# Kernel optimization log

Hardware: AMD Instinct MI355X
Metric: run time of the kernel (lower is better)

Reference implementation:

```python
import jax, jax.numpy as jnp
import numpy as np
from jax.scipy.linalg import expm

B, D, NF = 65536, 15, 199
DT, T_PERIOD, NORM = 0.05, 5.0, 150.0
TWO_PI = 2.0 * np.pi


def _pauli_s_const():
    # su(4) structure constants from normalized two-qubit Pauli basis G_a = (s_i x s_j)/2, Tr(Ga Gb)=delta
    I = np.eye(2, dtype=np.complex64)
    X = np.array([[0, 1], [1, 0]], np.complex64)
    Y = np.array([[0, -1j], [1j, 0]], np.complex64)
    Z = np.array([[1, 0], [0, -1]], np.complex64)
    P = [I, X, Y, Z]
    G = np.stack([np.kron(a, b) / 2.0 for i, a in enumerate(P) for j, b in enumerate(P) if (i, j) != (0, 0)])
    prod = np.einsum('aij,bjk->abik', G, G)
    comm = prod - prod.transpose(1, 0, 2, 3)
    anti = prod + prod.transpose(1, 0, 2, 3)
    f = np.real(-1j * np.einsum('abik,cki->abc', comm, G)).astype(np.float32)
    d = np.real(np.einsum('abik,cki->abc', anti, G)).astype(np.float32)
    return jnp.asarray(f), jnp.asarray(d)


def _fourier(t, freqs, amp):
    # FourierLayer: learnable frequencies + amplitudes, no phase; t: (B,1) -> (B, 2*NF)
    phase = TWO_PI * t * freqs / T_PERIOD  # (B, NF)
    return amp * jnp.concatenate([jnp.cos(phase), jnp.sin(phase)], axis=-1)


def setup_inputs() -> dict:
    key = jax.random.key(0)
    ks = jax.random.split(key, 12)
    t = jax.random.uniform(ks[0], (B, 1), jnp.float32) * T_PERIOD
    x = jax.random.normal(ks[1], (B, D), jnp.float32)
    # kaiming_uniform with a=10: bound = sqrt(6 / ((1 + a^2) * fan_in))
    bu = float(np.sqrt(6.0 / (101.0 * D)))
    u_re = jax.random.uniform(ks[2], (D, D), jnp.float32, -bu, bu)
    u_im = jax.random.uniform(ks[3], (D, D), jnp.float32, -bu, bu)
    freqs = jnp.arange(0.5, 100.0, 0.5, dtype=jnp.float32)  # (199,)
    bl = float(1.0 / np.sqrt(2 * NF))
    inp = {
        't': t, 'x': x, 'u_re': u_re, 'u_im': u_im,
        'freqs_g': freqs, 'amp_g': jnp.ones((2 * NF,), jnp.float32),
        'w_g': jax.random.uniform(ks[4], (D, 2 * NF), jnp.float32, -bl, bl),
        'b_g': jax.random.uniform(ks[5], (D,), jnp.float32, -bl, bl),
        'freqs_o': freqs, 'amp_o': jnp.ones((2 * NF,), jnp.float32),
        'w_o': jax.random.uniform(ks[6], (D, 2 * NF), jnp.float32, -bl, bl),
        'b_o': jax.random.uniform(ks[7], (D,), jnp.float32, -bl, bl),
    }
    f, d = _pauli_s_const()
    inp['f'] = f
    inp['d'] = d
    return inp


def reference(t, x, u_re, u_im, freqs_g, amp_g, w_g, b_g, freqs_o, amp_o, w_o, b_o, f, d):
    gamma = (( _fourier(t, freqs_g, amp_g) @ w_g.T + b_g) ** 2) / NORM   # (B, D), Square nonlin
    omega = (_fourier(t, freqs_o, amp_o) @ w_o.T + b_o) / NORM           # (B, D)
    # Hermitian theta -> unitary u = expm(i theta)
    theta = (u_re + u_re.T).astype(jnp.complex64) + 1j * (u_im - u_im.T).astype(jnp.complex64)
    u = expm(1j * theta)  # (D, D) complex64
    # Kossakowski matrix c = u diag(gamma) u^H, batched over samples
    c = jnp.einsum('ij,sj,lj->sil', u, gamma.astype(jnp.complex64), jnp.conj(u))
    c_re, c_im = c.real, c.imag
    dsx = (-4.0 * jnp.einsum('mjk,nik,sij->smn', f, f, c_re)
           - 4.0 * jnp.einsum('mik,njk,sij->smn', f, f, c_re)
           + 4.0 * jnp.einsum('mjk,nik,sij->smn', f, d, c_im)
           - 4.0 * jnp.einsum('mik,njk,sij->smn', f, d, c_im))
    tr_id = 4.0 * jnp.einsum('imj,sij->sm', f, c_im)
    h_comm = -4.0 * jnp.einsum('kij,sk->sij', f, omega)
    bsz = x.shape[0]
    L = jnp.zeros((bsz, D + 1, D + 1), jnp.float32)
    L = L.at[:, 1:, 1:].set(h_comm + dsx)
    L = L.at[:, 1:, 0].set(tr_id)
    E = jax.vmap(expm)(DT * L)  # batched 16x16 matrix exponential
    return E[:, 1:, 0] + jnp.einsum('si,sji->sj', x, E[:, 1:, 1:])
```

## Files before the change

### kernel.cpp

```cpp
#include <hip/hip_runtime.h>
#include <hip/hip_bf16.h>
#include <math.h>

#define NB      65536
#define DD      15
#define NFQ     199
#define DTC     0.05f
#define INV_NORM (1.0f/150.0f)
#define PH_SCALE 1.2566370614359172f
#define KTAY    10
#define KTAY_U  30

typedef _Float16 f16x8 __attribute__((ext_vector_type(8)));
typedef _Float16 f16x2 __attribute__((ext_vector_type(2)));
typedef float    f32x4 __attribute__((ext_vector_type(4)));

static __device__ __forceinline__ f16x2 u2h(unsigned u) {
    return __builtin_bit_cast(f16x2, u);
}
static __device__ __forceinline__ unsigned packh(float lo, float hi) {
    f16x2 h; h.x = (_Float16)lo; h.y = (_Float16)hi;
    return __builtin_bit_cast(unsigned, h);
}
static __device__ __forceinline__ f16x2 cvt_pk(float lo, float hi) {
    return __builtin_bit_cast(f16x2, __builtin_amdgcn_cvt_pkrtz(lo, hi));
}
static __device__ __forceinline__ float dot2(f16x2 cs, unsigned wbits, float acc) {
#if __has_builtin(__builtin_amdgcn_fdot2)
    return __builtin_amdgcn_fdot2(cs, u2h(wbits), acc, false);
#else
    f16x2 w = u2h(wbits);
    return acc + (float)cs.x * (float)w.x + (float)cs.y * (float)w.y;
#endif
}

__global__ __launch_bounds__(256) void k_pre(const float* __restrict__ u_re,
                                             const float* __restrict__ u_im,
                                             const float* __restrict__ ag,
                                             const float* __restrict__ wg,
                                             const float* __restrict__ ao,
                                             const float* __restrict__ wo,
                                             float* __restrict__ ws_u,
                                             unsigned* __restrict__ wt16) {
    int tid = threadIdx.x;
    if (blockIdx.x == 0) {
        __shared__ float Mre[225], Mim[225];
        __shared__ float cre[2][225], cim[2][225];
        float accre = 0.0f, accim = 0.0f;
        if (tid < 225) {
            int a = tid / 15, b = tid % 15;
            float tre = u_re[a*15+b] + u_re[b*15+a];
            float tim = u_im[a*15+b] - u_im[b*15+a];
            Mre[tid] = -tim;
            Mim[tid] =  tre;
            float id = (a == b) ? 1.0f : 0.0f;
            cre[0][tid] = id; cim[0][tid] = 0.0f;
            accre = id;
        }
        __syncthreads();
        int cur = 0;
        for (int k = 1; k <= KTAY_U; ++k) {
            float nre = 0.0f, nim = 0.0f;
            if (tid < 225) {
                int a = tid / 15, b = tid % 15;
                for (int j = 0; j < 15; ++j) {
                    float mre = Mre[a*15+j], mim = Mim[a*15+j];
                    float xre = cre[cur][j*15+b], xim = cim[cur][j*15+b];
                    nre += mre*xre - mim*xim;
                    nim += mre*xim + mim*xre;
                }
                float inv = 1.0f / (float)k;
                nre *= inv; nim *= inv;
                cre[cur^1][tid] = nre; cim[cur^1][tid] = nim;
                accre += nre; accim += nim;
            }
            __syncthreads();
            cur ^= 1;
        }
        if (tid < 225) {
            ws_u[2*tid]   = accre;
            ws_u[2*tid+1] = accim;
        }
    } else {
        int n = blockIdx.x - 1;
        if (tid < 32) {
            unsigned v = 0u;
            if (n < NFQ) {
                if (tid < 15) {
                    v = packh(wg[tid*398 + n] * ag[n],
                              wg[tid*398 + 199 + n] * ag[199 + n]);
                } else if (tid >= 16 && tid < 31) {
                    int m = tid - 16;
                    v = packh(wo[m*398 + n] * ao[n],
                              wo[m*398 + 199 + n] * ao[199 + n]);
                }
            }
            wt16[n*36 + tid] = v;
        }
    }
}

extern __shared__ float smem[];

__global__ __launch_bounds__(256) void k_mid(const float* __restrict__ f,
                                             const float* __restrict__ dten,
                                             const float* __restrict__ ws_u,
                                             const float* __restrict__ t,
                                             const float* __restrict__ bg,
                                             const float* __restrict__ bo,
                                             const unsigned* __restrict__ wt16,
                                             _Float16* __restrict__ Lb16,
                                             unsigned* __restrict__ coef16) {
    int tid = threadIdx.x;
    if (blockIdx.x < 16) {
        int p = blockIdx.x;
        int c = tid >> 4, r = tid & 15;
        if (p == 15) {
            Lb16[c*512 + r*32 + 15] = (_Float16)0.0f;
            Lb16[c*512 + r*32 + 31] = (_Float16)0.0f;
            return;
        }
        float* fsp  = smem;
        float* dshp = smem + 3600;
        float* FRt  = smem + 7200;
        float* DIt  = smem + 10800;
        float* Rm   = smem + 14400;
        float* Im   = smem + 14625;
        float* accA = smem + 14850;
        float* colv = smem + 15075;
        float* sur  = smem + 15090;
        float* sui  = smem + 15105;

        for (int idx = tid; idx < 3600; idx += 256) {
            int k = idx & 15, ab = idx >> 4;
            float fv = 0.0f, dv = 0.0f;
            if (k < 15) { fv = f[ab*15 + k]; dv = dten[ab*15 + k]; }
            fsp[idx] = fv; dshp[idx] = dv;
        }
        if (tid < 15) {
            sur[tid] = ws_u[2*(tid*15 + p)];
            sui[tid] = ws_u[2*(tid*15 + p) + 1];
        }
        __syncthreads();

        if (tid < 225) {
            int i = tid / 15, j = tid % 15;
            Rm[tid] = sur[i]*sur[j] + sui[i]*sui[j];
            Im[tid] = sui[i]*sur[j] - sur[i]*sui[j];
        }
        __syncthreads();

        for (int idx = tid; idx < 3600; idx += 256) {
            int k  = idx & 15;
            int nj = idx >> 4;
            int n  = nj / 15;
            int j  = nj % 15;
            float s1 = 0.0f, s2 = 0.0f;
            if (k < 15) {
                for (int i = 0; i < 15; ++i)  s1 += fsp[(n*15+i)*16 + k] * Rm[i*15 + j];
                for (int jj = 0; jj < 15; ++jj) s2 += dshp[(n*15+jj)*16 + k] * Im[j*15 + jj];
            }
            FRt[idx] = s1;
            DIt[idx] = s2;
        }
        __syncthreads();

        if (tid < 225) {
            int m = tid / 15, n = tid % 15;
            float acc = 0.0f;
            for (int j = 0; j < 15; ++j) {
                const float* fa = &fsp[(m*15+j)*16];
                const float* fb = &FRt[(n*15+j)*16];
                const float* fc = &DIt[(n*15+j)*16];
#pragma unroll
                for (int kk = 0; kk < 4; ++kk) {
                    float4 a4 = *(const float4*)(fa + 4*kk);
                    float4 b4 = *(const float4*)(fb + 4*kk);
                    float4 c4 = *(const float4*)(fc + 4*kk);
                    acc += a4.x*(b4.x + c4.x) + a4.y*(b4.y + c4.y)
                         + a4.z*(b4.z + c4.z) + a4.w*(b4.w + c4.w);
                }
            }
            accA[tid] = -8.0f * acc;
        }
        if (tid < 15) {
            int m = tid;
            float s = 0.0f;
            for (int i = 0; i < 15; ++i)
                for (int j = 0; j < 15; ++j)
                    s += fsp[(i*15+m)*16 + j] * Im[i*15 + j];
            colv[m] = 4.0f * s;
        }
        __syncthreads();

        float vg, vo;
        if (r == 0)      { vg = 0.0f;                      vo = 0.0f; }
        else if (c == 0) { vg = colv[r-1];                 vo = 0.0f; }
        else             { vg = accA[(r-1)*15 + (c-1)];
                           vo = -4.0f * fsp[(p*15 + (r-1))*16 + (c-1)]; }
        Lb16[c*512 + r*32 + p]      = (_Float16)vg;
        Lb16[c*512 + r*32 + 16 + p] = (_Float16)vo;
    } else {
        unsigned* lw = (unsigned*)smem;
        for (int idx = tid; idx < 200*32; idx += 256) {
            int n = idx >> 5, tt = idx & 31;
            lw[n*36 + tt] = wt16[n*36 + tt];
        }
        __syncthreads();

        int q = tid & 3;
        int p = tid >> 2;
        int sbase = (blockIdx.x - 16) * 256 + p;

        float rc[4], rs[4], rc4[4], rs4[4];
#pragma unroll
        for (int i = 0; i < 4; ++i) {
            float d = 0.5f * PH_SCALE * t[sbase + 64*i];
            __sincosf((float)(q + 1) * d, &rs[i], &rc[i]);
            __sincosf(4.0f * d, &rs4[i], &rc4[i]);
        }

        float ga[4][15], oa[4][15];
#pragma unroll
        for (int i = 0; i < 4; ++i)
#pragma unroll
            for (int m = 0; m < 15; ++m) { ga[i][m] = 0.0f; oa[i][m] = 0.0f; }

#pragma unroll 1
        for (int k = 0; k < 50; ++k) {
            const uint4* rowv = (const uint4*)(lw + (4*k + q) * 36);
            unsigned us[32];
#pragma unroll
            for (int j = 0; j < 8; ++j) {
                uint4 a_ = rowv[j];
                us[4*j] = a_.x; us[4*j+1] = a_.y; us[4*j+2] = a_.z; us[4*j+3] = a_.w;
            }
#pragma unroll
            for (int i = 0; i < 4; ++i) {
                f16x2 cs = cvt_pk(rc[i], rs[i]);
#pragma unroll
                for (int m = 0; m < 15; ++m) {
                    ga[i][m] = dot2(cs, us[m],      ga[i][m]);
                    oa[i][m] = dot2(cs, us[16 + m], oa[i][m]);
                }
                float cn = rc[i]*rc4[i] - rs[i]*rs4[i];
                float sn = rs[i]*rc4[i] + rc[i]*rs4[i];
                rc[i] = cn; rs[i] = sn;
            }
        }

#pragma unroll
        for (int i = 0; i < 4; ++i)
#pragma unroll
            for (int m = 0; m < 15; ++m) {
                ga[i][m] += __shfl_xor(ga[i][m], 1, 64);
                ga[i][m] += __shfl_xor(ga[i][m], 2, 64);
                oa[i][m] += __shfl_xor(oa[i][m], 1, 64);
                oa[i][m] += __shfl_xor(oa[i][m], 2, 64);
            }

        float bgv[15], bov[15];
#pragma unroll
        for (int m = 0; m < 15; ++m) { bgv[m] = bg[m]; bov[m] = bo[m]; }

#pragma unroll
        for (int i = 0; i < 4; ++i) {
            float rv[32];
#pragma unroll
            for (int m = 0; m < 15; ++m) {
                float g = ga[i][m] + bgv[m];
                rv[m]      = g * g * INV_NORM;
                rv[16 + m] = (oa[i][m] + bov[m]) * INV_NORM;
            }
            rv[15] = 0.0f; rv[31] = 0.0f;
            unsigned u0  = packh(rv[0],  rv[1]),  u1  = packh(rv[2],  rv[3]);
            unsigned u2  = packh(rv[4],  rv[5]),  u3  = packh(rv[6],  rv[7]);
            unsigned u4  = packh(rv[8],  rv[9]),  u5  = packh(rv[10], rv[11]);
            unsigned u6  = packh(rv[12], rv[13]), u7  = packh(rv[14], rv[15]);
            unsigned u8  = packh(rv[16], rv[17]), u9  = packh(rv[18], rv[19]);
            unsigned u10 = packh(rv[20], rv[21]), u11 = packh(rv[22], rv[23]);
            unsigned u12 = packh(rv[24], rv[25]), u13 = packh(rv[26], rv[27]);
            unsigned u14 = packh(rv[28], rv[29]), u15 = packh(rv[30], rv[31]);
            uint4 wr;
            if      (q == 0) wr = make_uint4(u0,  u1,  u2,  u3);
            else if (q == 1) wr = make_uint4(u4,  u5,  u6,  u7);
            else if (q == 2) wr = make_uint4(u8,  u9,  u10, u11);
            else             wr = make_uint4(u12, u13, u14, u15);
            *(uint4*)(coef16 + (size_t)(sbase + 64*i) * 16 + 4*q) = wr;
        }
    }
}

__global__ __launch_bounds__(256) void k_main(const float* __restrict__ x,
                                              const unsigned* __restrict__ coef16,
                                              const _Float16* __restrict__ Lb16,
                                              float* __restrict__ out) {
    __shared__ float wl[4 * 16 * 20];
    int tid  = threadIdx.x;
    int wave = tid >> 6, lane = tid & 63;
    int grp  = lane >> 4, sl = lane & 15;
    int s    = blockIdx.x * 64 + wave * 16 + sl;

    f16x8 bh = *(const f16x8*)((const _Float16*)coef16 + (size_t)s * 32 + grp * 8);

    f32x4 acc[16];
    f32x4 zero4 = {0.0f, 0.0f, 0.0f, 0.0f};
#pragma unroll
    for (int c = 0; c < 16; ++c) {
        f16x8 af = *(const f16x8*)(Lb16 + c*512 + sl*32 + grp*8);
        acc[c] = __builtin_amdgcn_mfma_f32_16x16x32_f16(af, bh, zero4, 0, 0, 0);
    }

    float4 wv;
    if (grp == 0) {
        const float* xp = x + (size_t)s * 15;
        wv = make_float4(1.0f, xp[0], xp[1], xp[2]);
    } else {
        const float* xp = x + (size_t)s * 15 + 4*grp - 1;
        wv = make_float4(xp[0], xp[1], xp[2], xp[3]);
    }
    float4 accv = wv;

    float* slot = wl + wave*320 + sl*20;
#pragma unroll
    for (int k = 1; k <= KTAY; ++k) {
        *(float4*)(slot + 4*grp) = wv;
        float wz[16];
        {
            float4 a = *(const float4*)(slot + 0);
            wz[0]=a.x; wz[1]=a.y; wz[2]=a.z; wz[3]=a.w;
            float4 b = *(const float4*)(slot + 4);
            wz[4]=b.x; wz[5]=b.y; wz[6]=b.z; wz[7]=b.w;
            float4 c = *(const float4*)(slot + 8);
            wz[8]=c.x; wz[9]=c.y; wz[10]=c.z; wz[11]=c.w;
            float4 d = *(const float4*)(slot + 12);
            wz[12]=d.x; wz[13]=d.y; wz[14]=d.z; wz[15]=d.w;
        }
        float nx = 0.0f, ny = 0.0f, nz = 0.0f, nw = 0.0f;
#pragma unroll
        for (int c = 0; c < 16; ++c) {
            f32x4 A = acc[c];
            float wc = wz[c];
            nx += A.x * wc; ny += A.y * wc; nz += A.z * wc; nw += A.w * wc;
        }
        float sc = DTC / (float)k;
        wv = make_float4(nx*sc, ny*sc, nz*sc, nw*sc);
        accv.x += wv.x; accv.y += wv.y; accv.z += wv.z; accv.w += wv.w;
    }

    float* op = out + (size_t)s * 15 - 1;
    int row = 4 * grp;
    if (row > 0)     op[row]     = accv.x;
    op[row + 1] = accv.y;
    op[row + 2] = accv.z;
    op[row + 3] = accv.w;
}

extern "C" void kernel_launch(void* const* d_in, const int* in_sizes, int n_in,
                              void* d_out, int out_size, void* d_ws, size_t ws_size,
                              hipStream_t stream) {
    const float* t    = (const float*)d_in[0];
    const float* x    = (const float*)d_in[1];
    const float* u_re = (const float*)d_in[2];
    const float* u_im = (const float*)d_in[3];
    const float* ag   = (const float*)d_in[5];
    const float* wg   = (const float*)d_in[6];
    const float* bg   = (const float*)d_in[7];
    const float* ao   = (const float*)d_in[9];
    const float* wo   = (const float*)d_in[10];
    const float* bo   = (const float*)d_in[11];
    const float* f    = (const float*)d_in[12];
    const float* dten = (const float*)d_in[13];
    float* out = (float*)d_out;
    float* ws  = (float*)d_ws;

    float*     u_ws   = ws;
    _Float16*  Lb16   = (_Float16*)(ws + 512);
    unsigned*  wt16   = (unsigned*)(ws + 4608);
    unsigned*  coef16 = (unsigned*)(ws + 12288);

    hipLaunchKernelGGL(k_pre,  dim3(201),  dim3(256), 0,     stream,
                       u_re, u_im, ag, wg, ao, wo, u_ws, wt16);
    hipLaunchKernelGGL(k_mid,  dim3(272),  dim3(256), 60480, stream,
                       f, dten, u_ws, t, bg, bo, wt16, Lb16, coef16);
    hipLaunchKernelGGL(k_main, dim3(1024), dim3(256), 0,     stream,
                       x, coef16, Lb16, out);
}
```

Before: 140.8 us.

## Fuse three kernels into one cooperative kernel with a grid-wide sync

Replaces the three-launch pipeline (pre, mid, main) with a single cooperative kernel of 256 blocks. The first 16 blocks each compute the unitary exponential redundantly, with the Taylor order cut from 30 to 18, and then build the generator matrices from fp16-packed structure constants. The remaining blocks build the Fourier weights in shared memory and loop over sample chunks to compute the coefficients. After a grid.sync, every block runs the batched MFMA Taylor exponential for its 256 samples, so launch gaps and intermediate workspace round trips go away. In exchange the grid is smaller and stalls at the grid barrier. Fewer Taylor terms and fp16 constants also add precision risk, and the old three kernels are kept as a fallback if the cooperative launch fails.

```diff
diff --git a/kernel.cpp b/kernel.cpp
--- a/kernel.cpp
+++ b/kernel.cpp
@@ -1,15 +1,17 @@
 #include <hip/hip_runtime.h>
+#include <hip/hip_cooperative_groups.h>
 #include <hip/hip_bf16.h>
 #include <math.h>
 
+namespace cg = cooperative_groups;
+
 #define NB      65536
-#define DD      15
 #define NFQ     199
 #define DTC     0.05f
 #define INV_NORM (1.0f/150.0f)
 #define PH_SCALE 1.2566370614359172f
 #define KTAY    10
-#define KTAY_U  30
+#define KTAY_U  18
 
 typedef _Float16 f16x8 __attribute__((ext_vector_type(8)));
 typedef _Float16 f16x2 __attribute__((ext_vector_type(2)));
@@ -32,6 +34,307 @@
     f16x2 w = u2h(wbits);
     return acc + (float)cs.x * (float)w.x + (float)cs.y * (float)w.y;
 #endif
+}
+
+extern __shared__ float sm[];
+
+__global__ __launch_bounds__(256) void k_all(
+        const float* __restrict__ t,   const float* __restrict__ x,
+        const float* __restrict__ u_re,const float* __restrict__ u_im,
+        const float* __restrict__ ag,  const float* __restrict__ wg,
+        const float* __restrict__ bg,  const float* __restrict__ ao,
+        const float* __restrict__ wo,  const float* __restrict__ bo,
+        const float* __restrict__ f,   const float* __restrict__ dten,
+        _Float16* __restrict__ Lb16,   unsigned* __restrict__ coef16,
+        float* __restrict__ out) {
+    int tid = threadIdx.x;
+    int bid = blockIdx.x;
+
+    if (bid < 16) {
+        if (bid == 15) {
+            int c = tid >> 4, r = tid & 15;
+            Lb16[c*512 + r*32 + 15] = (_Float16)0.0f;
+            Lb16[c*512 + r*32 + 31] = (_Float16)0.0f;
+        } else {
+            int p = bid;
+            unsigned* fd16 = (unsigned*)sm;
+            float* S    = sm + 3600;
+            float* Rm   = sm + 7200;
+            float* Im   = sm + 7425;
+            float* accA = sm + 7650;
+            float* colv = sm + 7875;
+            float* sur  = sm + 7890;
+            float* sui  = sm + 7905;
+            float* Mre  = sm + 3600;
+            float* Mim  = sm + 3825;
+            float* creb = sm + 4050;
+            float* cimb = sm + 4500;
+
+            for (int idx = tid; idx < 3600; idx += 256) {
+                int k = idx & 15, ab = idx >> 4;
+                float fv = 0.0f, dv = 0.0f;
+                if (k < 15) { fv = f[ab*15 + k]; dv = dten[ab*15 + k]; }
+                fd16[idx] = packh(fv, dv);
+            }
+            float accre = 0.0f, accim = 0.0f;
+            if (tid < 225) {
+                int a = tid / 15, b = tid % 15;
+                float tre = u_re[a*15+b] + u_re[b*15+a];
+                float tim = u_im[a*15+b] - u_im[b*15+a];
+                Mre[tid] = -tim;
+                Mim[tid] =  tre;
+                float id = (a == b) ? 1.0f : 0.0f;
+                creb[tid] = id; cimb[tid] = 0.0f;
+                accre = id;
+            }
+            __syncthreads();
+            int cur = 0;
+            for (int k = 1; k <= KTAY_U; ++k) {
+                float nre = 0.0f, nim = 0.0f;
+                if (tid < 225) {
+                    int a = tid / 15, b = tid % 15;
+                    for (int j = 0; j < 15; ++j) {
+                        float mre = Mre[a*15+j], mim = Mim[a*15+j];
+                        float xre = creb[cur*225 + j*15+b], xim = cimb[cur*225 + j*15+b];
+                        nre += mre*xre - mim*xim;
+                        nim += mre*xim + mim*xre;
+                    }
+                    float inv = 1.0f / (float)k;
+                    nre *= inv; nim *= inv;
+                    creb[(cur^1)*225 + tid] = nre; cimb[(cur^1)*225 + tid] = nim;
+                    accre += nre; accim += nim;
+                }
+                __syncthreads();
+                cur ^= 1;
+            }
+            if (tid < 225 && (tid % 15) == p) { sur[tid/15] = accre; sui[tid/15] = accim; }
+            __syncthreads();
+            if (tid < 225) {
+                int i = tid / 15, j = tid % 15;
+                Rm[tid] = sur[i]*sur[j] + sui[i]*sui[j];
+                Im[tid] = sui[i]*sur[j] - sur[i]*sui[j];
+            }
+            __syncthreads();
+            for (int idx = tid; idx < 3600; idx += 256) {
+                int k  = idx & 15;
+                int nj = idx >> 4;
+                int n  = nj / 15;
+                int j  = nj % 15;
+                float s1 = 0.0f, s2 = 0.0f;
+                if (k < 15) {
+                    for (int i = 0; i < 15; ++i) {
+                        f16x2 fd = u2h(fd16[(n*15+i)*16 + k]);
+                        s1 += (float)fd.x * Rm[i*15 + j];
+                        s2 += (float)fd.y * Im[j*15 + i];
+                    }
+                }
+                S[idx] = s1 + s2;
+            }
+            __syncthreads();
+            if (tid < 225) {
+                int m = tid / 15, n = tid % 15;
+                float acc = 0.0f;
+                for (int j = 0; j < 15; ++j) {
+                    const unsigned* fa = &fd16[(m*15+j)*16];
+                    const float*    fs = &S   [(n*15+j)*16];
+                    for (int k = 0; k < 15; ++k) {
+                        f16x2 fd = u2h(fa[k]);
+                        acc += (float)fd.x * fs[k];
+                    }
+                }
+                accA[tid] = -8.0f * acc;
+            }
+            if (tid < 15) {
+                int m = tid;
+                float s = 0.0f;
+                for (int i = 0; i < 15; ++i)
+                    for (int j = 0; j < 15; ++j) {
+                        f16x2 fd = u2h(fd16[(i*15+m)*16 + j]);
+                        s += (float)fd.x * Im[i*15 + j];
+                    }
+                colv[m] = 4.0f * s;
+            }
+            __syncthreads();
+            {
+                int c = tid >> 4, r = tid & 15;
+                float vg, vo;
+                if (r == 0)      { vg = 0.0f;              vo = 0.0f; }
+                else if (c == 0) { vg = colv[r-1];         vo = 0.0f; }
+                else             { vg = accA[(r-1)*15 + (c-1)];
+                                   f16x2 fd = u2h(fd16[(p*15 + (r-1))*16 + (c-1)]);
+                                   vo = -4.0f * (float)fd.x; }
+                Lb16[c*512 + r*32 + p]      = (_Float16)vg;
+                Lb16[c*512 + r*32 + 16 + p] = (_Float16)vo;
+            }
+        }
+    } else {
+        unsigned* lw = (unsigned*)sm;
+        for (int idx = tid; idx < 200*36; idx += 256) lw[idx] = 0u;
+        __syncthreads();
+        for (int idx = tid; idx < 15*200; idx += 256) {
+            int m = idx / 200, n = idx % 200;
+            if (n < NFQ)
+                lw[n*36 + m] = packh(wg[m*398 + n]       * ag[n],
+                                     wg[m*398 + 199 + n] * ag[199 + n]);
+        }
+        for (int idx = tid; idx < 15*200; idx += 256) {
+            int m = idx / 200, n = idx % 200;
+            if (n < NFQ)
+                lw[n*36 + 16 + m] = packh(wo[m*398 + n]       * ao[n],
+                                          wo[m*398 + 199 + n] * ao[199 + n]);
+        }
+        __syncthreads();
+
+        int q = tid & 3;
+        int pp = tid >> 2;
+
+        float bgv[15], bov[15];
+#pragma unroll
+        for (int m = 0; m < 15; ++m) { bgv[m] = bg[m]; bov[m] = bo[m]; }
+
+        for (int cb = bid - 16; cb < 256; cb += 240) {
+            int sbase = cb * 256 + pp;
+
+            float rc[4], rs[4], rc4[4], rs4[4];
+#pragma unroll
+            for (int i = 0; i < 4; ++i) {
+                float d = 0.5f * PH_SCALE * t[sbase + 64*i];
+                __sincosf((float)(q + 1) * d, &rs[i], &rc[i]);
+                __sincosf(4.0f * d, &rs4[i], &rc4[i]);
+            }
+
+            float ga[4][15], oa[4][15];
+#pragma unroll
+            for (int i = 0; i < 4; ++i)
+#pragma unroll
+                for (int m = 0; m < 15; ++m) { ga[i][m] = 0.0f; oa[i][m] = 0.0f; }
+
+#pragma unroll 1
+            for (int k = 0; k < 50; ++k) {
+                const uint4* rowv = (const uint4*)(lw + (4*k + q) * 36);
+                unsigned us[32];
+#pragma unroll
+                for (int j = 0; j < 8; ++j) {
+                    uint4 a_ = rowv[j];
+                    us[4*j] = a_.x; us[4*j+1] = a_.y; us[4*j+2] = a_.z; us[4*j+3] = a_.w;
+                }
+#pragma unroll
+                for (int i = 0; i < 4; ++i) {
+                    f16x2 cs = cvt_pk(rc[i], rs[i]);
+#pragma unroll
+                    for (int m = 0; m < 15; ++m) {
+                        ga[i][m] = dot2(cs, us[m],      ga[i][m]);
+                        oa[i][m] = dot2(cs, us[16 + m], oa[i][m]);
+                    }
+                    float cn = rc[i]*rc4[i] - rs[i]*rs4[i];
+                    float sn = rs[i]*rc4[i] + rc[i]*rs4[i];
+                    rc[i] = cn; rs[i] = sn;
+                }
+            }
+
+#pragma unroll
+            for (int i = 0; i < 4; ++i)
+#pragma unroll
+                for (int m = 0; m < 15; ++m) {
+                    ga[i][m] += __shfl_xor(ga[i][m], 1, 64);
+                    ga[i][m] += __shfl_xor(ga[i][m], 2, 64);
+                    oa[i][m] += __shfl_xor(oa[i][m], 1, 64);
+                    oa[i][m] += __shfl_xor(oa[i][m], 2, 64);
+                }
+
+#pragma unroll
+            for (int i = 0; i < 4; ++i) {
+                float rv[32];
+#pragma unroll
+                for (int m = 0; m < 15; ++m) {
+                    float g = ga[i][m] + bgv[m];
+                    rv[m]      = g * g * INV_NORM;
+                    rv[16 + m] = (oa[i][m] + bov[m]) * INV_NORM;
+                }
+                rv[15] = 0.0f; rv[31] = 0.0f;
+                unsigned u0  = packh(rv[0],  rv[1]),  u1  = packh(rv[2],  rv[3]);
+                unsigned u2  = packh(rv[4],  rv[5]),  u3  = packh(rv[6],  rv[7]);
+                unsigned u4  = packh(rv[8],  rv[9]),  u5  = packh(rv[10], rv[11]);
+                unsigned u6  = packh(rv[12], rv[13]), u7  = packh(rv[14], rv[15]);
+                unsigned u8  = packh(rv[16], rv[17]), u9  = packh(rv[18], rv[19]);
+                unsigned u10 = packh(rv[20], rv[21]), u11 = packh(rv[22], rv[23]);
+                unsigned u12 = packh(rv[24], rv[25]), u13 = packh(rv[26], rv[27]);
+                unsigned u14 = packh(rv[28], rv[29]), u15 = packh(rv[30], rv[31]);
+                uint4 wr;
+                if      (q == 0) wr = make_uint4(u0,  u1,  u2,  u3);
+                else if (q == 1) wr = make_uint4(u4,  u5,  u6,  u7);
+                else if (q == 2) wr = make_uint4(u8,  u9,  u10, u11);
+                else             wr = make_uint4(u12, u13, u14, u15);
+                *(uint4*)(coef16 + (size_t)(sbase + 64*i) * 16 + 4*q) = wr;
+            }
+        }
+    }
+
+    __threadfence();
+    cg::this_grid().sync();
+
+    float* wl = sm;
+    int wave = tid >> 6, lane = tid & 63;
+    int grp  = lane >> 4, sl = lane & 15;
+    f32x4 zero4 = {0.0f, 0.0f, 0.0f, 0.0f};
+    float* slot = wl + wave*320 + sl*20;
+
+#pragma unroll 1
+    for (int pass = 0; pass < 4; ++pass) {
+        int s = (bid << 8) + (pass << 6) + (wave << 4) + sl;
+
+        f16x8 bh = *(const f16x8*)((const _Float16*)coef16 + (size_t)s * 32 + grp * 8);
+
+        f32x4 acc[16];
+#pragma unroll
+        for (int c = 0; c < 16; ++c) {
+            f16x8 af = *(const f16x8*)(Lb16 + c*512 + sl*32 + grp*8);
+            acc[c] = __builtin_amdgcn_mfma_f32_16x16x32_f16(af, bh, zero4, 0, 0, 0);
+        }
+
+        float4 wv;
+        if (grp == 0) {
+            const float* xp = x + (size_t)s * 15;
+            wv = make_float4(1.0f, xp[0], xp[1], xp[2]);
+        } else {
+            const float* xp = x + (size_t)s * 15 + 4*grp - 1;
+            wv = make_float4(xp[0], xp[1], xp[2], xp[3]);
+        }
+        float4 accv = wv;
+
+#pragma unroll
+        for (int k = 1; k <= KTAY; ++k) {
+            *(float4*)(slot + 4*grp) = wv;
+            float wz[16];
+            {
+                float4 a = *(const float4*)(slot + 0);
+                wz[0]=a.x; wz[1]=a.y; wz[2]=a.z; wz[3]=a.w;
+                float4 b = *(const float4*)(slot + 4);
+                wz[4]=b.x; wz[5]=b.y; wz[6]=b.z; wz[7]=b.w;
+                float4 c = *(const float4*)(slot + 8);
+                wz[8]=c.x; wz[9]=c.y; wz[10]=c.z; wz[11]=c.w;
+                float4 d = *(const float4*)(slot + 12);
+                wz[12]=d.x; wz[13]=d.y; wz[14]=d.z; wz[15]=d.w;
+            }
+            float nx = 0.0f, ny = 0.0f, nz = 0.0f, nw = 0.0f;
+#pragma unroll
+            for (int c = 0; c < 16; ++c) {
+                f32x4 A = acc[c];
+                float wc = wz[c];
+                nx += A.x * wc; ny += A.y * wc; nz += A.z * wc; nw += A.w * wc;
+            }
+            float sc = DTC / (float)k;
+            wv = make_float4(nx*sc, ny*sc, nz*sc, nw*sc);
+            accv.x += wv.x; accv.y += wv.y; accv.z += wv.z; accv.w += wv.w;
+        }
+
+        float* op = out + (size_t)s * 15 - 1;
+        int row = 4 * grp;
+        if (row > 0) op[row] = accv.x;
+        op[row + 1] = accv.y;
+        op[row + 2] = accv.z;
+        op[row + 3] = accv.w;
+    }
 }
 
 __global__ __launch_bounds__(256) void k_pre(const float* __restrict__ u_re,
@@ -59,7 +362,7 @@
         }
         __syncthreads();
         int cur = 0;
-        for (int k = 1; k <= KTAY_U; ++k) {
+        for (int k = 1; k <= 30; ++k) {
             float nre = 0.0f, nim = 0.0f;
             if (tid < 225) {
                 int a = tid / 15, b = tid % 15;
@@ -99,8 +402,6 @@
         }
     }
 }
-
-extern __shared__ float smem[];
 
 __global__ __launch_bounds__(256) void k_mid(const float* __restrict__ f,
                                              const float* __restrict__ dten,
@@ -120,16 +421,16 @@
             Lb16[c*512 + r*32 + 31] = (_Float16)0.0f;
             return;
         }
-        float* fsp  = smem;
-        float* dshp = smem + 3600;
-        float* FRt  = smem + 7200;
-        float* DIt  = smem + 10800;
-        float* Rm   = smem + 14400;
-        float* Im   = smem + 14625;
-        float* accA = smem + 14850;
-        float* colv = smem + 15075;
-        float* sur  = smem + 15090;
-        float* sui  = smem + 15105;
+        float* fsp  = sm;
+        float* dshp = sm + 3600;
+        float* FRt  = sm + 7200;
+        float* DIt  = sm + 10800;
+        float* Rm   = sm + 14400;
+        float* Im   = sm + 14625;
+        float* accA = sm + 14850;
+        float* colv = sm + 15075;
+        float* sur  = sm + 15090;
+        float* sui  = sm + 15105;
 
         for (int idx = tid; idx < 3600; idx += 256) {
             int k = idx & 15, ab = idx >> 4;
@@ -194,14 +495,16 @@
         __syncthreads();
 
         float vg, vo;
-        if (r == 0)      { vg = 0.0f;                      vo = 0.0f; }
-        else if (c == 0) { vg = colv[r-1];                 vo = 0.0f; }
+        if (r == 0)      { vg = 0.0f;              vo = 0.0f; }
+        else if (c == 0) { vg = colv[r-1];         vo = 0.0f; }
         else             { vg = accA[(r-1)*15 + (c-1)];
                            vo = -4.0f * fsp[(p*15 + (r-1))*16 + (c-1)]; }
         Lb16[c*512 + r*32 + p]      = (_Float16)vg;
         Lb16[c*512 + r*32 + 16 + p] = (_Float16)vo;
     } else {
-        unsigned* lw = (unsigned*)smem;
+        unsigned* lw = (unsigned*)sm;
+        for (int idx = tid; idx < 200*36; idx += 256) lw[idx] = 0u;
+        __syncthreads();
         for (int idx = tid; idx < 200*32; idx += 256) {
             int n = idx >> 5, tt = idx & 31;
             lw[n*36 + tt] = wt16[n*36 + tt];
@@ -209,8 +512,8 @@
         __syncthreads();
 
         int q = tid & 3;
-        int p = tid >> 2;
-        int sbase = (blockIdx.x - 16) * 256 + p;
+        int pp = tid >> 2;
+        int sbase = (blockIdx.x - 16) * 256 + pp;
 
         float rc[4], rs[4], rc4[4], rs4[4];
 #pragma unroll
@@ -350,7 +653,7 @@
 
     float* op = out + (size_t)s * 15 - 1;
     int row = 4 * grp;
-    if (row > 0)     op[row]     = accv.x;
+    if (row > 0) op[row] = accv.x;
     op[row + 1] = accv.y;
     op[row + 2] = accv.z;
     op[row + 3] = accv.w;
@@ -374,15 +677,27 @@
     float* out = (float*)d_out;
     float* ws  = (float*)d_ws;
 
-    float*     u_ws   = ws;
-    _Float16*  Lb16   = (_Float16*)(ws + 512);
-    unsigned*  wt16   = (unsigned*)(ws + 4608);
-    unsigned*  coef16 = (unsigned*)(ws + 12288);
-
-    hipLaunchKernelGGL(k_pre,  dim3(201),  dim3(256), 0,     stream,
-                       u_re, u_im, ag, wg, ao, wo, u_ws, wt16);
-    hipLaunchKernelGGL(k_mid,  dim3(272),  dim3(256), 60480, stream,
-                       f, dten, u_ws, t, bg, bo, wt16, Lb16, coef16);
-    hipLaunchKernelGGL(k_main, dim3(1024), dim3(256), 0,     stream,
-                       x, coef16, Lb16, out);
-}
+    float*    u_ws   = ws;
+    _Float16* Lb16   = (_Float16*)(ws + 512);
+    unsigned* wt16   = (unsigned*)(ws + 4608);
+    unsigned* coef16 = (unsigned*)(ws + 12288);
+
+    void* args[] = {
+        (void*)&t, (void*)&x, (void*)&u_re, (void*)&u_im,
+        (void*)&ag, (void*)&wg, (void*)&bg,
+        (void*)&ao, (void*)&wo, (void*)&bo,
+        (void*)&f, (void*)&dten,
+        (void*)&Lb16, (void*)&coef16, (void*)&out
+    };
+    hipError_t err = hipLaunchCooperativeKernel((const void*)k_all,
+                                                dim3(256), dim3(256),
+                                                args, 31744, stream);
+    if (err != hipSuccess) {
+        hipLaunchKernelGGL(k_pre,  dim3(201),  dim3(256), 0,     stream,
+                           u_re, u_im, ag, wg, ao, wo, u_ws, wt16);
+        hipLaunchKernelGGL(k_mid,  dim3(272),  dim3(256), 60480, stream,
+                           f, dten, u_ws, t, bg, bo, wt16, Lb16, coef16);
+        hipLaunchKernelGGL(k_main, dim3(1024), dim3(256), 0,     stream,
+                           x, coef16, Lb16, out);
+    }
+}
```

After: 221.8 us. 1.58x slower.

## Merge pre and mid kernels, recompute expm per block, halve Fourier loop

Applied to the files above, without the earlier changes.

Folds the prologue and middle kernels into a single launch. Each L-building block now recomputes the 15x15 unitary exponential itself with fewer Taylor terms, and every Fourier block repacks the weights into shared memory directly, so the workspace round trip and one kernel launch go away. Shared memory is cut by storing f and d packed as fp16 pairs and merging the FR/DI scratch. The Fourier stage now splits each sample over 8 lanes instead of 4, using twice as many blocks with a shorter frequency loop and an extra shuffle level. The trade-offs are redundant expm work in 15 blocks, lower precision in the truncated series and fp16 structure constants, and a repack of the weights in every Fourier block.

```diff
diff --git a/kernel.cpp b/kernel.cpp
--- a/kernel.cpp
+++ b/kernel.cpp
@@ -3,13 +3,12 @@
 #include <math.h>
 
 #define NB      65536
-#define DD      15
 #define NFQ     199
 #define DTC     0.05f
 #define INV_NORM (1.0f/150.0f)
 #define PH_SCALE 1.2566370614359172f
 #define KTAY    10
-#define KTAY_U  30
+#define KTAY_U  18
 
 typedef _Float16 f16x8 __attribute__((ext_vector_type(8)));
 typedef _Float16 f16x2 __attribute__((ext_vector_type(2)));
@@ -34,190 +33,164 @@
 #endif
 }
 
-__global__ __launch_bounds__(256) void k_pre(const float* __restrict__ u_re,
-                                             const float* __restrict__ u_im,
-                                             const float* __restrict__ ag,
-                                             const float* __restrict__ wg,
-                                             const float* __restrict__ ao,
-                                             const float* __restrict__ wo,
-                                             float* __restrict__ ws_u,
-                                             unsigned* __restrict__ wt16) {
+extern __shared__ float sm[];
+
+__global__ __launch_bounds__(256) void k_A(
+        const float* __restrict__ t,
+        const float* __restrict__ u_re,const float* __restrict__ u_im,
+        const float* __restrict__ ag,  const float* __restrict__ wg,
+        const float* __restrict__ bg,  const float* __restrict__ ao,
+        const float* __restrict__ wo,  const float* __restrict__ bo,
+        const float* __restrict__ f,   const float* __restrict__ dten,
+        _Float16* __restrict__ Lb16,   unsigned* __restrict__ coef16) {
     int tid = threadIdx.x;
-    if (blockIdx.x == 0) {
-        __shared__ float Mre[225], Mim[225];
-        __shared__ float cre[2][225], cim[2][225];
-        float accre = 0.0f, accim = 0.0f;
-        if (tid < 225) {
-            int a = tid / 15, b = tid % 15;
-            float tre = u_re[a*15+b] + u_re[b*15+a];
-            float tim = u_im[a*15+b] - u_im[b*15+a];
-            Mre[tid] = -tim;
-            Mim[tid] =  tre;
-            float id = (a == b) ? 1.0f : 0.0f;
-            cre[0][tid] = id; cim[0][tid] = 0.0f;
-            accre = id;
-        }
-        __syncthreads();
-        int cur = 0;
-        for (int k = 1; k <= KTAY_U; ++k) {
-            float nre = 0.0f, nim = 0.0f;
+    int bid = blockIdx.x;
+
+    if (bid < 16) {
+        if (bid == 15) {
+            int c = tid >> 4, r = tid & 15;
+            Lb16[c*512 + r*32 + 15] = (_Float16)0.0f;
+            Lb16[c*512 + r*32 + 31] = (_Float16)0.0f;
+        } else {
+            int p = bid;
+            unsigned* fd16 = (unsigned*)sm;
+            float* S    = sm + 3600;
+            float* Rm   = sm + 7200;
+            float* Im   = sm + 7425;
+            float* accA = sm + 7650;
+            float* colv = sm + 7875;
+            float* sur  = sm + 7890;
+            float* sui  = sm + 7905;
+            float* Mre  = sm + 3600;
+            float* Mim  = sm + 3825;
+            float* creb = sm + 4050;
+            float* cimb = sm + 4500;
+
+            for (int idx = tid; idx < 3600; idx += 256) {
+                int k = idx & 15, ab = idx >> 4;
+                float fv = 0.0f, dv = 0.0f;
+                if (k < 15) { fv = f[ab*15 + k]; dv = dten[ab*15 + k]; }
+                fd16[idx] = packh(fv, dv);
+            }
+            float accre = 0.0f, accim = 0.0f;
             if (tid < 225) {
                 int a = tid / 15, b = tid % 15;
+                float tre = u_re[a*15+b] + u_re[b*15+a];
+                float tim = u_im[a*15+b] - u_im[b*15+a];
+                Mre[tid] = -tim;
+                Mim[tid] =  tre;
+                float id = (a == b) ? 1.0f : 0.0f;
+                creb[tid] = id; cimb[tid] = 0.0f;
+                accre = id;
+            }
+            __syncthreads();
+            int cur = 0;
+            for (int k = 1; k <= KTAY_U; ++k) {
+                float nre = 0.0f, nim = 0.0f;
+                if (tid < 225) {
+                    int a = tid / 15, b = tid % 15;
+                    for (int j = 0; j < 15; ++j) {
+                        float mre = Mre[a*15+j], mim = Mim[a*15+j];
+                        float xre = creb[cur*225 + j*15+b], xim = cimb[cur*225 + j*15+b];
+                        nre += mre*xre - mim*xim;
+                        nim += mre*xim + mim*xre;
+                    }
+                    float inv = 1.0f / (float)k;
+                    nre *= inv; nim *= inv;
+                    creb[(cur^1)*225 + tid] = nre; cimb[(cur^1)*225 + tid] = nim;
+                    accre += nre; accim += nim;
+                }
+                __syncthreads();
+                cur ^= 1;
+            }
+            if (tid < 225 && (tid % 15) == p) { sur[tid/15] = accre; sui[tid/15] = accim; }
+            __syncthreads();
+            if (tid < 225) {
+                int i = tid / 15, j = tid % 15;
+                Rm[tid] = sur[i]*sur[j] + sui[i]*sui[j];
+                Im[tid] = sui[i]*sur[j] - sur[i]*sui[j];
+            }
+            __syncthreads();
+            for (int idx = tid; idx < 3600; idx += 256) {
+                int k  = idx & 15;
+                int nj = idx >> 4;
+                int n  = nj / 15;
+                int j  = nj % 15;
+                float s1 = 0.0f, s2 = 0.0f;
+                if (k < 15) {
+                    for (int i = 0; i < 15; ++i) {
+                        f16x2 fd = u2h(fd16[(n*15+i)*16 + k]);
+                        s1 += (float)fd.x * Rm[i*15 + j];
+                        s2 += (float)fd.y * Im[j*15 + i];
+                    }
+                }
+                S[idx] = s1 + s2;
+            }
+            __syncthreads();
+            if (tid < 225) {
+                int m = tid / 15, n = tid % 15;
+                float acc = 0.0f;
                 for (int j = 0; j < 15; ++j) {
-                    float mre = Mre[a*15+j], mim = Mim[a*15+j];
-                    float xre = cre[cur][j*15+b], xim = cim[cur][j*15+b];
-                    nre += mre*xre - mim*xim;
-                    nim += mre*xim + mim*xre;
+                    const unsigned* fa = &fd16[(m*15+j)*16];
+                    const float*    fs = &S   [(n*15+j)*16];
+                    for (int k = 0; k < 15; ++k) {
+                        f16x2 fd = u2h(fa[k]);
+                        acc += (float)fd.x * fs[k];
+                    }
                 }
-                float inv = 1.0f / (float)k;
-                nre *= inv; nim *= inv;
-                cre[cur^1][tid] = nre; cim[cur^1][tid] = nim;
-                accre += nre; accim += nim;
-            }
-            __syncthreads();
-            cur ^= 1;
-        }
-        if (tid < 225) {
-            ws_u[2*tid]   = accre;
-            ws_u[2*tid+1] = accim;
+                accA[tid] = -8.0f * acc;
+            }
+            if (tid < 15) {
+                int m = tid;
+                float s = 0.0f;
+                for (int i = 0; i < 15; ++i)
+                    for (int j = 0; j < 15; ++j) {
+                        f16x2 fd = u2h(fd16[(i*15+m)*16 + j]);
+                        s += (float)fd.x * Im[i*15 + j];
+                    }
+                colv[m] = 4.0f * s;
+            }
+            __syncthreads();
+            {
+                int c = tid >> 4, r = tid & 15;
+                float vg, vo;
+                if (r == 0)      { vg = 0.0f;              vo = 0.0f; }
+                else if (c == 0) { vg = colv[r-1];         vo = 0.0f; }
+                else             { vg = accA[(r-1)*15 + (c-1)];
+                                   f16x2 fd = u2h(fd16[(p*15 + (r-1))*16 + (c-1)]);
+                                   vo = -4.0f * (float)fd.x; }
+                Lb16[c*512 + r*32 + p]      = (_Float16)vg;
+                Lb16[c*512 + r*32 + 16 + p] = (_Float16)vo;
+            }
         }
     } else {
-        int n = blockIdx.x - 1;
-        if (tid < 32) {
-            unsigned v = 0u;
-            if (n < NFQ) {
-                if (tid < 15) {
-                    v = packh(wg[tid*398 + n] * ag[n],
-                              wg[tid*398 + 199 + n] * ag[199 + n]);
-                } else if (tid >= 16 && tid < 31) {
-                    int m = tid - 16;
-                    v = packh(wo[m*398 + n] * ao[n],
-                              wo[m*398 + 199 + n] * ao[199 + n]);
-                }
-            }
-            wt16[n*36 + tid] = v;
-        }
-    }
-}
-
-extern __shared__ float smem[];
-
-__global__ __launch_bounds__(256) void k_mid(const float* __restrict__ f,
-                                             const float* __restrict__ dten,
-                                             const float* __restrict__ ws_u,
-                                             const float* __restrict__ t,
-                                             const float* __restrict__ bg,
-                                             const float* __restrict__ bo,
-                                             const unsigned* __restrict__ wt16,
-                                             _Float16* __restrict__ Lb16,
-                                             unsigned* __restrict__ coef16) {
-    int tid = threadIdx.x;
-    if (blockIdx.x < 16) {
-        int p = blockIdx.x;
-        int c = tid >> 4, r = tid & 15;
-        if (p == 15) {
-            Lb16[c*512 + r*32 + 15] = (_Float16)0.0f;
-            Lb16[c*512 + r*32 + 31] = (_Float16)0.0f;
-            return;
-        }
-        float* fsp  = smem;
-        float* dshp = smem + 3600;
-        float* FRt  = smem + 7200;
-        float* DIt  = smem + 10800;
-        float* Rm   = smem + 14400;
-        float* Im   = smem + 14625;
-        float* accA = smem + 14850;
-        float* colv = smem + 15075;
-        float* sur  = smem + 15090;
-        float* sui  = smem + 15105;
-
-        for (int idx = tid; idx < 3600; idx += 256) {
-            int k = idx & 15, ab = idx >> 4;
-            float fv = 0.0f, dv = 0.0f;
-            if (k < 15) { fv = f[ab*15 + k]; dv = dten[ab*15 + k]; }
-            fsp[idx] = fv; dshp[idx] = dv;
-        }
-        if (tid < 15) {
-            sur[tid] = ws_u[2*(tid*15 + p)];
-            sui[tid] = ws_u[2*(tid*15 + p) + 1];
-        }
+        unsigned* lw = (unsigned*)sm;
+        for (int idx = tid; idx < 200*36; idx += 256) lw[idx] = 0u;
         __syncthreads();
-
-        if (tid < 225) {
-            int i = tid / 15, j = tid % 15;
-            Rm[tid] = sur[i]*sur[j] + sui[i]*sui[j];
-            Im[tid] = sui[i]*sur[j] - sur[i]*sui[j];
+        for (int idx = tid; idx < 15*200; idx += 256) {
+            int m = idx / 200, n = idx % 200;
+            if (n < NFQ)
+                lw[n*36 + m] = packh(wg[m*398 + n]       * ag[n],
+                                     wg[m*398 + 199 + n] * ag[199 + n]);
+        }
+        for (int idx = tid; idx < 15*200; idx += 256) {
+            int m = idx / 200, n = idx % 200;
+            if (n < NFQ)
+                lw[n*36 + 16 + m] = packh(wo[m*398 + n]       * ao[n],
+                                          wo[m*398 + 199 + n] * ao[199 + n]);
         }
         __syncthreads();
 
-        for (int idx = tid; idx < 3600; idx += 256) {
-            int k  = idx & 15;
-            int nj = idx >> 4;
-            int n  = nj / 15;
-            int j  = nj % 15;
-            float s1 = 0.0f, s2 = 0.0f;
-            if (k < 15) {
-                for (int i = 0; i < 15; ++i)  s1 += fsp[(n*15+i)*16 + k] * Rm[i*15 + j];
-                for (int jj = 0; jj < 15; ++jj) s2 += dshp[(n*15+jj)*16 + k] * Im[j*15 + jj];
-            }
-            FRt[idx] = s1;
-            DIt[idx] = s2;
-        }
-        __syncthreads();
-
-        if (tid < 225) {
-            int m = tid / 15, n = tid % 15;
-            float acc = 0.0f;
-            for (int j = 0; j < 15; ++j) {
-                const float* fa = &fsp[(m*15+j)*16];
-                const float* fb = &FRt[(n*15+j)*16];
-                const float* fc = &DIt[(n*15+j)*16];
-#pragma unroll
-                for (int kk = 0; kk < 4; ++kk) {
-                    float4 a4 = *(const float4*)(fa + 4*kk);
-                    float4 b4 = *(const float4*)(fb + 4*kk);
-                    float4 c4 = *(const float4*)(fc + 4*kk);
-                    acc += a4.x*(b4.x + c4.x) + a4.y*(b4.y + c4.y)
-                         + a4.z*(b4.z + c4.z) + a4.w*(b4.w + c4.w);
-                }
-            }
-            accA[tid] = -8.0f * acc;
-        }
-        if (tid < 15) {
-            int m = tid;
-            float s = 0.0f;
-            for (int i = 0; i < 15; ++i)
-                for (int j = 0; j < 15; ++j)
-                    s += fsp[(i*15+m)*16 + j] * Im[i*15 + j];
-            colv[m] = 4.0f * s;
-        }
-        __syncthreads();
-
-        float vg, vo;
-        if (r == 0)      { vg = 0.0f;                      vo = 0.0f; }
-        else if (c == 0) { vg = colv[r-1];                 vo = 0.0f; }
-        else             { vg = accA[(r-1)*15 + (c-1)];
-                           vo = -4.0f * fsp[(p*15 + (r-1))*16 + (c-1)]; }
-        Lb16[c*512 + r*32 + p]      = (_Float16)vg;
-        Lb16[c*512 + r*32 + 16 + p] = (_Float16)vo;
-    } else {
-        unsigned* lw = (unsigned*)smem;
-        for (int idx = tid; idx < 200*32; idx += 256) {
-            int n = idx >> 5, tt = idx & 31;
-            lw[n*36 + tt] = wt16[n*36 + tt];
-        }
-        __syncthreads();
-
-        int q = tid & 3;
-        int p = tid >> 2;
-        int sbase = (blockIdx.x - 16) * 256 + p;
-
-        float rc[4], rs[4], rc4[4], rs4[4];
+        int q  = tid & 7;
+        int pp = tid >> 3;
+        int sbase = (bid - 16) * 128 + pp;
+
+        float rc[4], rs[4], rc8[4], rs8[4];
 #pragma unroll
         for (int i = 0; i < 4; ++i) {
-            float d = 0.5f * PH_SCALE * t[sbase + 64*i];
+            float d = 0.5f * PH_SCALE * t[sbase + 32*i];
             __sincosf((float)(q + 1) * d, &rs[i], &rc[i]);
-            __sincosf(4.0f * d, &rs4[i], &rc4[i]);
+            __sincosf(8.0f * d, &rs8[i], &rc8[i]);
         }
 
         float ga[4][15], oa[4][15];
@@ -227,8 +200,8 @@
             for (int m = 0; m < 15; ++m) { ga[i][m] = 0.0f; oa[i][m] = 0.0f; }
 
 #pragma unroll 1
-        for (int k = 0; k < 50; ++k) {
-            const uint4* rowv = (const uint4*)(lw + (4*k + q) * 36);
+        for (int k = 0; k < 25; ++k) {
+            const uint4* rowv = (const uint4*)(lw + (8*k + q) * 36);
             unsigned us[32];
 #pragma unroll
             for (int j = 0; j < 8; ++j) {
@@ -243,8 +216,8 @@
                     ga[i][m] = dot2(cs, us[m],      ga[i][m]);
                     oa[i][m] = dot2(cs, us[16 + m], oa[i][m]);
                 }
-                float cn = rc[i]*rc4[i] - rs[i]*rs4[i];
-                float sn = rs[i]*rc4[i] + rc[i]*rs4[i];
+                float cn = rc[i]*rc8[i] - rs[i]*rs8[i];
+                float sn = rs[i]*rc8[i] + rc[i]*rs8[i];
                 rc[i] = cn; rs[i] = sn;
             }
         }
@@ -255,8 +228,10 @@
             for (int m = 0; m < 15; ++m) {
                 ga[i][m] += __shfl_xor(ga[i][m], 1, 64);
                 ga[i][m] += __shfl_xor(ga[i][m], 2, 64);
+                ga[i][m] += __shfl_xor(ga[i][m], 4, 64);
                 oa[i][m] += __shfl_xor(oa[i][m], 1, 64);
                 oa[i][m] += __shfl_xor(oa[i][m], 2, 64);
+                oa[i][m] += __shfl_xor(oa[i][m], 4, 64);
             }
 
         float bgv[15], bov[15];
@@ -273,20 +248,13 @@
                 rv[16 + m] = (oa[i][m] + bov[m]) * INV_NORM;
             }
             rv[15] = 0.0f; rv[31] = 0.0f;
-            unsigned u0  = packh(rv[0],  rv[1]),  u1  = packh(rv[2],  rv[3]);
-            unsigned u2  = packh(rv[4],  rv[5]),  u3  = packh(rv[6],  rv[7]);
-            unsigned u4  = packh(rv[8],  rv[9]),  u5  = packh(rv[10], rv[11]);
-            unsigned u6  = packh(rv[12], rv[13]), u7  = packh(rv[14], rv[15]);
-            unsigned u8  = packh(rv[16], rv[17]), u9  = packh(rv[18], rv[19]);
-            unsigned u10 = packh(rv[20], rv[21]), u11 = packh(rv[22], rv[23]);
-            unsigned u12 = packh(rv[24], rv[25]), u13 = packh(rv[26], rv[27]);
-            unsigned u14 = packh(rv[28], rv[29]), u15 = packh(rv[30], rv[31]);
-            uint4 wr;
-            if      (q == 0) wr = make_uint4(u0,  u1,  u2,  u3);
-            else if (q == 1) wr = make_uint4(u4,  u5,  u6,  u7);
-            else if (q == 2) wr = make_uint4(u8,  u9,  u10, u11);
-            else             wr = make_uint4(u12, u13, u14, u15);
-            *(uint4*)(coef16 + (size_t)(sbase + 64*i) * 16 + 4*q) = wr;
+            if (q < 4) {
+                uint4 wr = make_uint4(packh(rv[8*q+0], rv[8*q+1]),
+                                      packh(rv[8*q+2], rv[8*q+3]),
+                                      packh(rv[8*q+4], rv[8*q+5]),
+                                      packh(rv[8*q+6], rv[8*q+7]));
+                *(uint4*)(coef16 + (size_t)(sbase + 32*i) * 16 + 4*q) = wr;
+            }
         }
     }
 }
@@ -350,7 +318,7 @@
 
     float* op = out + (size_t)s * 15 - 1;
     int row = 4 * grp;
-    if (row > 0)     op[row]     = accv.x;
+    if (row > 0) op[row] = accv.x;
     op[row + 1] = accv.y;
     op[row + 2] = accv.z;
     op[row + 3] = accv.w;
@@ -372,17 +340,13 @@
     const float* f    = (const float*)d_in[12];
     const float* dten = (const float*)d_in[13];
     float* out = (float*)d_out;
-    float* ws  = (float*)d_ws;
-
-    float*     u_ws   = ws;
-    _Float16*  Lb16   = (_Float16*)(ws + 512);
-    unsigned*  wt16   = (unsigned*)(ws + 4608);
-    unsigned*  coef16 = (unsigned*)(ws + 12288);
-
-    hipLaunchKernelGGL(k_pre,  dim3(201),  dim3(256), 0,     stream,
-                       u_re, u_im, ag, wg, ao, wo, u_ws, wt16);
-    hipLaunchKernelGGL(k_mid,  dim3(272),  dim3(256), 60480, stream,
-                       f, dten, u_ws, t, bg, bo, wt16, Lb16, coef16);
+
+    _Float16* Lb16   = (_Float16*)d_ws;
+    unsigned* coef16 = (unsigned*)((char*)d_ws + 16384);
+
+    hipLaunchKernelGGL(k_A,    dim3(528),  dim3(256), 31744, stream,
+                       t, u_re, u_im, ag, wg, bg, ao, wo, bo, f, dten,
+                       Lb16, coef16);
     hipLaunchKernelGGL(k_main, dim3(1024), dim3(256), 0,     stream,
                        x, coef16, Lb16, out);
 }
```

After: 160.9 us. +14.3%, slower.
